# Kernel tuning notes

Hardware: AMD Instinct MI355X
Metric: run time of the kernel (lower is better)

Reference implementation:

```python
import jax, jax.numpy as jnp
import numpy as np

N, K, C, H, V = 4096, 32, 128, 128, 21   # residues, kNN, node/edge dim, hidden, vocab
NEG_SLOPE = 0.2

def gatv2(src_feat, tgt_feat, edge_feat, Wl, bl, Wr, br, We, be, att, b_out):
    # GATv2Conv (1 head, eval mode) on a regular kNN graph.
    # src_feat: [N,K,Din] gathered source-node features per edge; tgt_feat: [N,Din]
    xl = src_feat @ Wl + bl                       # [N,K,C]
    xr = tgt_feat @ Wr + br                       # [N,C]
    ee = edge_feat @ We + be                      # [N,K,C]
    m = jax.nn.leaky_relu(xl + xr[:, None, :] + ee, NEG_SLOPE)
    alpha = jax.nn.softmax(jnp.einsum('nkc,c->nk', m, att), axis=1)
    return jnp.einsum('nk,nkc->nc', alpha, xl) + b_out

def setup_inputs():
    key = jax.random.key(0)
    ks = jax.random.split(key, 32)
    w = lambda k, s: jax.random.normal(k, s, jnp.float32) * 0.05
    z0 = lambda s: jnp.zeros(s, jnp.float32)
    return dict(
        E=jax.random.normal(ks[0], (N, K, C), jnp.float32),
        E_idx=jax.random.randint(ks[1], (N, K), 0, N),
        S=jax.random.randint(ks[2], (N,), 0, V),
        mask=jnp.ones((N,), jnp.float32),
        chain_M=jnp.ones((N,), jnp.float32),
        z=jax.random.normal(ks[3], (N,), jnp.float32),
        Wl1=w(ks[4], (C, C)), bl1=z0((C,)),
        Wr1=w(ks[5], (C, C)), br1=z0((C,)),
        We1=w(ks[6], (C, C)), be1=z0((C,)),
        a1=w(ks[7], (C,)), bo1=z0((C,)),
        Wl2=w(ks[8], (C + H, C)), bl2=z0((C,)),
        Wr2=w(ks[9], (C + H, C)), br2=z0((C,)),
        We2=w(ks[10], (C, C)), be2=z0((C,)),
        a2=w(ks[11], (C,)), bo2=z0((C,)),
        W_s=w(ks[12], (V, H)),
        W_out=w(ks[13], (C, V)), b_out=z0((V,)),
    )

def reference(E, E_idx, S, mask, chain_M, z,
              Wl1, bl1, Wr1, br1, We1, be1, a1, bo1,
              Wl2, bl2, Wr2, br2, We2, be2, a2, bo2,
              W_s, W_out, b_out):
    # encoder GAT over zero-initialized node features
    x0 = jnp.zeros((N, C), E.dtype)
    node_attr = gatv2(x0[E_idx], x0, E, Wl1, bl1, Wr1, br1, We1, be1, a1, bo1)
    seq_attr = W_s[S]                                        # [N,H]
    h_full = jnp.concatenate([node_attr, seq_attr], -1)      # [N,C+H]
    h_mask = jnp.concatenate([node_attr, jnp.zeros_like(seq_attr)], -1)
    cm = chain_M * mask
    decoding_order = jnp.argsort((cm + 1e-4) * jnp.abs(z))   # [N]
    P = jax.nn.one_hot(decoding_order, N, dtype=E.dtype)     # [N,N] permutation
    L = 1.0 - jnp.triu(jnp.ones((N, N), E.dtype))            # strictly lower tri
    order_mask_backward = jnp.einsum('ij,iq,jp->qp', L, P, P)
    mask_attend = jnp.take_along_axis(order_mask_backward, E_idx, axis=1)[..., None]
    m1d = mask[:, None, None]
    mask_bw = m1d * mask_attend
    mask_fw = m1d * (1.0 - mask_attend)
    # per-edge source features: neighbor seq embedding visible only if decoded earlier
    src = h_full[E_idx] * mask_bw + h_mask[E_idx] * mask_fw  # [N,K,C+H]
    out = gatv2(src, h_mask, E, Wl2, bl2, Wr2, br2, We2, be2, a2, bo2)
    logits = out @ W_out + b_out
    return jax.nn.log_softmax(logits, axis=-1)
```

## Files before the change

### kernel.cpp

```cpp
#include <hip/hip_runtime.h>
#include <hip/hip_bf16.h>

typedef short short8 __attribute__((ext_vector_type(8)));
typedef float float4v __attribute__((ext_vector_type(4)));

#define WS_T   0
#define WS_D   2688
#define WS_C   2816
#define WS_O   2944
#define WS_A2  3072
#define WS_G   7296
#define WS_B0  7744
#define WS_B1  7776
#define WS_M   7808

__device__ __forceinline__ unsigned int pack2bf(float a, float b) {
  union { float f; unsigned int u; } xa, xb;
  xa.f = a; xb.f = b;
  return ((xa.u + 0x8000u) >> 16) | ((xb.u + 0x8000u) & 0xFFFF0000u);
}

__global__ __launch_bounds__(256) void pg10_pre(
    const float* __restrict__ Wl2, const float* __restrict__ Wr2,
    const float* __restrict__ We2, const float* __restrict__ bl1,
    const float* __restrict__ bl2, const float* __restrict__ br2,
    const float* __restrict__ be2, const float* __restrict__ a2,
    const float* __restrict__ bo1, const float* __restrict__ bo2,
    const float* __restrict__ W_s, const float* __restrict__ mask,
    const float* __restrict__ chain_M, const float* __restrict__ z,
    const int* __restrict__ S, const float* __restrict__ W_out,
    const float* __restrict__ b_out, void* __restrict__ ws)
{
  __shared__ float sA[128], sB[128];
  short* wsW = (short*)ws;
  float* F = (float*)ws + 8192;
  const int b = blockIdx.x, tid = threadIdx.x;
  if (b == 0) {
    for (int s = tid; s < 16384; s += 256) {
      const int row = s >> 7, c = s & 127;
      const int q = row >> 5, lh = (row & 31) >> 3, j = row & 7;
      const int t = c >> 4, cl = c & 15;
      union { float f; unsigned int u; } x; x.f = We2[s];
      const unsigned int r = x.u + 0x7FFFu + ((x.u >> 16) & 1u);
      wsW[(((q * 8 + t) * 64) + lh * 16 + cl) * 8 + j] = (short)(r >> 16);
    }
    if (tid < 128) {
      const int c = tid;
      float cl0 = 0.f, cr0 = 0.f;
      for (int i = 0; i < 128; i++) {
        const float s = bl1[i] + bo1[i];
        cl0 += s * Wl2[i * 128 + c];
        cr0 += s * Wr2[i * 128 + c];
      }
      const float O = bl2[c] + bo2[c];
      F[WS_D + c]  = be2[c] + bl2[c] + br2[c] + cr0;
      F[WS_C + c]  = cl0;
      F[WS_O + c]  = O;
      F[WS_A2 + c] = a2[c];
      sA[c] = O;
      sB[c] = cl0;
    }
    __syncthreads();
    if (tid < 21) {
      float b0 = b_out[tid], b1 = 0.f;
      for (int c = 0; c < 128; c++) {
        b0 = fmaf(sA[c], W_out[c * 21 + tid], b0);
        b1 = fmaf(sB[c], W_out[c * 21 + tid], b1);
      }
      F[WS_B0 + tid] = b0;
      F[WS_B1 + tid] = b1;
    }
  } else if (b <= 21) {
    const int v = b - 1;
    if (tid < 128) {
      const int c = tid;
      float acc = 0.f;
      for (int h = 0; h < 128; h++)
        acc += W_s[v * 128 + h] * Wl2[(128 + h) * 128 + c];
      F[WS_T + v * 128 + c] = acc;
      sA[c] = acc;
    }
    __syncthreads();
    if (tid < 21) {
      float g = 0.f;
      for (int c = 0; c < 128; c++)
        g = fmaf(sA[c], W_out[c * 21 + tid], g);
      F[WS_G + v * 21 + tid] = g;
    }
  } else {
    const int n = (b - 22) * 256 + tid;
    F[WS_M + 2 * n] = (chain_M[n] * mask[n] + 1e-4f) * fabsf(z[n]);
    ((int*)F)[WS_M + 2 * n + 1] = S[n];
  }
}

__global__ __launch_bounds__(256, 4) void pg10_main(
    const float* __restrict__ E, const int* __restrict__ E_idx,
    const float* __restrict__ mask, const void* __restrict__ ws,
    float* __restrict__ out)
{
  __shared__ __align__(16) short ldsE[4][32 * 136];

  const short* wsW = (const short*)ws;
  const float* F = (const float*)ws + 8192;
  const int tid  = threadIdx.x;
  const int wave = tid >> 6;
  const int lane = tid & 63;
  const int quad = lane >> 4;
  const int lid  = lane & 15;
  const int n    = blockIdx.x * 4 + wave;
  const float maskn = mask[n];

  int jidx = 0;
  if (lane < 32) jidx = E_idx[n * 32 + lane];

  const float* ebase = E + (size_t)n * 32 * 128;
  short* myE = ldsE[wave];
#pragma unroll
  for (int i = 0; i < 8; i++) {
    const int e = i * 512 + lane * 8;
    const float4 A = *(const float4*)(ebase + e);
    const float4 B = *(const float4*)(ebase + e + 4);
    union { short8 s; unsigned int u[4]; } v;
    v.u[0] = pack2bf(A.x, A.y);
    v.u[1] = pack2bf(A.z, A.w);
    v.u[2] = pack2bf(B.x, B.y);
    v.u[3] = pack2bf(B.z, B.w);
    *(short8*)(myE + (e >> 7) * 136 + (e & 127)) = v.s;
  }

  float wkv = 0.f; int rvv = 0;
  const float keyn = F[WS_M + 2 * n];
  if (lane < 32) {
    const float2 mj = *(const float2*)(F + WS_M + 2 * jidx);
    const int before = (mj.x < keyn) || (mj.x == keyn && jidx < n);
    wkv = before ? maskn : 0.f;
    union { float f; int i; } c; c.f = mj.y; rvv = c.i;
  }
  int rows[2][4]; float wks[2][4];
#pragma unroll
  for (int g = 0; g < 2; g++)
#pragma unroll
    for (int r = 0; r < 4; r++) {
      const int kk = g * 16 + quad * 4 + r;
      rows[g][r] = __shfl(rvv, kk) * 128;
      wks[g][r]  = __shfl(wkv, kk);
    }

  __builtin_amdgcn_wave_barrier();

  short8 afr[2][4];
#pragma unroll
  for (int g = 0; g < 2; g++)
#pragma unroll
    for (int q = 0; q < 4; q++)
      afr[g][q] = *(const short8*)(myE + (g * 16 + lid) * 136 + q * 32 + quad * 8);

  float part[2][4] = {{0.f, 0.f, 0.f, 0.f}, {0.f, 0.f, 0.f, 0.f}};
#pragma unroll
  for (int t = 0; t < 8; t++) {
    short8 bfr[4];
#pragma unroll
    for (int q = 0; q < 4; q++)
      bfr[q] = *(const short8*)(wsW + (((q * 8 + t) * 64) + lane) * 8);
    float4v ac0 = {0.f, 0.f, 0.f, 0.f}, ac1 = {0.f, 0.f, 0.f, 0.f};
#pragma unroll
    for (int q = 0; q < 4; q++) {
      ac0 = __builtin_amdgcn_mfma_f32_16x16x32_bf16(afr[0][q], bfr[q], ac0, 0, 0, 0);
      ac1 = __builtin_amdgcn_mfma_f32_16x16x32_bf16(afr[1][q], bfr[q], ac1, 0, 0, 0);
    }
    const int c = t * 16 + lid;
    const float dvt  = F[WS_D + c] + maskn * F[WS_C + c];
    const float a2vt = F[WS_A2 + c];
#pragma unroll
    for (int r = 0; r < 4; r++) {
      float v0 = ac0[r] + dvt + wks[0][r] * F[WS_T + rows[0][r] + c];
      float v1 = ac1[r] + dvt + wks[1][r] * F[WS_T + rows[1][r] + c];
      v0 = fmaxf(v0, 0.f) + 0.2f * fminf(v0, 0.f);
      v1 = fmaxf(v1, 0.f) + 0.2f * fminf(v1, 0.f);
      part[0][r] = fmaf(v0, a2vt, part[0][r]);
      part[1][r] = fmaf(v1, a2vt, part[1][r]);
    }
  }
  float sreg[2][4];
#pragma unroll
  for (int g = 0; g < 2; g++)
#pragma unroll
    for (int r = 0; r < 4; r++) {
      float v = part[g][r];
      v += __shfl_xor(v, 1);
      v += __shfl_xor(v, 2);
      v += __shfl_xor(v, 4);
      v += __shfl_xor(v, 8);
      sreg[g][r] = v;
    }

  float mx = -1e30f;
#pragma unroll
  for (int g = 0; g < 2; g++)
#pragma unroll
    for (int r = 0; r < 4; r++) mx = fmaxf(mx, sreg[g][r]);
  mx = fmaxf(mx, __shfl_xor(mx, 16));
  mx = fmaxf(mx, __shfl_xor(mx, 32));
  float eg[2][4], esum = 0.f;
#pragma unroll
  for (int g = 0; g < 2; g++)
#pragma unroll
    for (int r = 0; r < 4; r++) {
      eg[g][r] = expf(sreg[g][r] - mx);
      esum += eg[g][r];
    }
  esum += __shfl_xor(esum, 16);
  esum += __shfl_xor(esum, 32);
  const float inv = 1.f / esum;
  float cg[2][4];
#pragma unroll
  for (int g = 0; g < 2; g++)
#pragma unroll
    for (int r = 0; r < 4; r++) cg[g][r] = eg[g][r] * inv * wks[g][r];

  float lg = (lane < 21) ? (F[WS_B0 + lane] + maskn * F[WS_B1 + lane]) : -1e30f;
#pragma unroll
  for (int kk = 0; kk < 32; kk++) {
    const int g = kk >> 4, sq = (kk >> 2) & 3, r = kk & 3;
    const float cf = __shfl(cg[g][r], sq * 16);
    const int row = (rows[0][0], __shfl(rvv, kk)) * 21;
    if (lane < 21) lg = fmaf(cf, F[WS_G + row + lane], lg);
  }

  float lmx = lg;
  lmx = fmaxf(lmx, __shfl_xor(lmx, 1));
  lmx = fmaxf(lmx, __shfl_xor(lmx, 2));
  lmx = fmaxf(lmx, __shfl_xor(lmx, 4));
  lmx = fmaxf(lmx, __shfl_xor(lmx, 8));
  lmx = fmaxf(lmx, __shfl_xor(lmx, 16));
  float ex = (lane < 21) ? expf(lg - lmx) : 0.f;
  float es = ex;
  es += __shfl_xor(es, 1);
  es += __shfl_xor(es, 2);
  es += __shfl_xor(es, 4);
  es += __shfl_xor(es, 8);
  es += __shfl_xor(es, 16);
  if (lane < 21)
    out[n * 21 + lane] = lg - lmx - logf(es);
}

extern "C" void kernel_launch(void* const* d_in, const int* in_sizes, int n_in,
                              void* d_out, int out_size, void* d_ws, size_t ws_size,
                              hipStream_t stream)
{
  const float* E       = (const float*)d_in[0];
  const int*   E_idx   = (const int*)d_in[1];
  const int*   S       = (const int*)d_in[2];
  const float* mask    = (const float*)d_in[3];
  const float* chain_M = (const float*)d_in[4];
  const float* z       = (const float*)d_in[5];
  const float* bl1     = (const float*)d_in[7];
  const float* bo1     = (const float*)d_in[13];
  const float* Wl2     = (const float*)d_in[14];
  const float* bl2     = (const float*)d_in[15];
  const float* Wr2     = (const float*)d_in[16];
  const float* br2     = (const float*)d_in[17];
  const float* We2     = (const float*)d_in[18];
  const float* be2     = (const float*)d_in[19];
  const float* a2      = (const float*)d_in[20];
  const float* bo2     = (const float*)d_in[21];
  const float* W_s     = (const float*)d_in[22];
  const float* W_out   = (const float*)d_in[23];
  const float* b_out   = (const float*)d_in[24];

  pg10_pre<<<38, 256, 0, stream>>>(Wl2, Wr2, We2, bl1, bl2, br2, be2, a2,
                                   bo1, bo2, W_s, mask, chain_M, z, S,
                                   W_out, b_out, d_ws);
  pg10_main<<<1024, 256, 0, stream>>>(E, E_idx, mask, d_ws, (float*)d_out);
}
```

Before: 168.2 us.

## Use intrinsic bf16 packing, hoist per-channel constants, split logit accumulation

Replaces the hand-written round-half-up bf16 packing of E with the HIP __float22bfloat162_rn intrinsic, which rounds to nearest even and may map to a packed convert instruction. Hoists the per-channel bias and attention-vector loads out of the MFMA loop into register arrays. Splits the 32-step logit accumulation into two independent FMA chains to shorten the dependency chain. These add register pressure under a 4-blocks-per-SM launch bound, and the rounding change slightly alters numerics.

```diff
diff --git a/kernel.cpp b/kernel.cpp
--- a/kernel.cpp
+++ b/kernel.cpp
@@ -14,13 +14,18 @@
 #define WS_B1  7776
 #define WS_M   7808
 
-__device__ __forceinline__ unsigned int pack2bf(float a, float b) {
-  union { float f; unsigned int u; } xa, xb;
-  xa.f = a; xb.f = b;
-  return ((xa.u + 0x8000u) >> 16) | ((xb.u + 0x8000u) & 0xFFFF0000u);
-}
-
-__global__ __launch_bounds__(256) void pg10_pre(
+__device__ __forceinline__ ushort f2bf(float f) {
+  union { float f; unsigned int u; } x;
+  x.f = f;
+  unsigned int r = x.u + 0x7FFFu + ((x.u >> 16) & 1u);
+  return (ushort)(r >> 16);
+}
+__device__ __forceinline__ unsigned int pkbf(float a, float b) {
+  __hip_bfloat162 h = __float22bfloat162_rn(make_float2(a, b));
+  return *(unsigned int*)&h;
+}
+
+__global__ __launch_bounds__(256) void pg12_pre(
     const float* __restrict__ Wl2, const float* __restrict__ Wr2,
     const float* __restrict__ We2, const float* __restrict__ bl1,
     const float* __restrict__ bl2, const float* __restrict__ br2,
@@ -40,9 +45,7 @@
       const int row = s >> 7, c = s & 127;
       const int q = row >> 5, lh = (row & 31) >> 3, j = row & 7;
       const int t = c >> 4, cl = c & 15;
-      union { float f; unsigned int u; } x; x.f = We2[s];
-      const unsigned int r = x.u + 0x7FFFu + ((x.u >> 16) & 1u);
-      wsW[(((q * 8 + t) * 64) + lh * 16 + cl) * 8 + j] = (short)(r >> 16);
+      wsW[(((q * 8 + t) * 64) + lh * 16 + cl) * 8 + j] = (short)f2bf(We2[s]);
     }
     if (tid < 128) {
       const int c = tid;
@@ -94,7 +97,7 @@
   }
 }
 
-__global__ __launch_bounds__(256, 4) void pg10_main(
+__global__ __launch_bounds__(256, 4) void pg12_main(
     const float* __restrict__ E, const int* __restrict__ E_idx,
     const float* __restrict__ mask, const void* __restrict__ ws,
     float* __restrict__ out)
@@ -122,10 +125,10 @@
     const float4 A = *(const float4*)(ebase + e);
     const float4 B = *(const float4*)(ebase + e + 4);
     union { short8 s; unsigned int u[4]; } v;
-    v.u[0] = pack2bf(A.x, A.y);
-    v.u[1] = pack2bf(A.z, A.w);
-    v.u[2] = pack2bf(B.x, B.y);
-    v.u[3] = pack2bf(B.z, B.w);
+    v.u[0] = pkbf(A.x, A.y);
+    v.u[1] = pkbf(A.z, A.w);
+    v.u[2] = pkbf(B.x, B.y);
+    v.u[3] = pkbf(B.z, B.w);
     *(short8*)(myE + (e >> 7) * 136 + (e & 127)) = v.s;
   }
 
@@ -147,6 +150,14 @@
       wks[g][r]  = __shfl(wkv, kk);
     }
 
+  float dv[8], a2v[8];
+#pragma unroll
+  for (int t = 0; t < 8; t++) {
+    const int c = t * 16 + lid;
+    dv[t]  = F[WS_D + c] + maskn * F[WS_C + c];
+    a2v[t] = F[WS_A2 + c];
+  }
+
   __builtin_amdgcn_wave_barrier();
 
   short8 afr[2][4];
@@ -170,16 +181,14 @@
       ac1 = __builtin_amdgcn_mfma_f32_16x16x32_bf16(afr[1][q], bfr[q], ac1, 0, 0, 0);
     }
     const int c = t * 16 + lid;
-    const float dvt  = F[WS_D + c] + maskn * F[WS_C + c];
-    const float a2vt = F[WS_A2 + c];
-#pragma unroll
-    for (int r = 0; r < 4; r++) {
-      float v0 = ac0[r] + dvt + wks[0][r] * F[WS_T + rows[0][r] + c];
-      float v1 = ac1[r] + dvt + wks[1][r] * F[WS_T + rows[1][r] + c];
+#pragma unroll
+    for (int r = 0; r < 4; r++) {
+      float v0 = ac0[r] + dv[t] + wks[0][r] * F[WS_T + rows[0][r] + c];
+      float v1 = ac1[r] + dv[t] + wks[1][r] * F[WS_T + rows[1][r] + c];
       v0 = fmaxf(v0, 0.f) + 0.2f * fminf(v0, 0.f);
       v1 = fmaxf(v1, 0.f) + 0.2f * fminf(v1, 0.f);
-      part[0][r] = fmaf(v0, a2vt, part[0][r]);
-      part[1][r] = fmaf(v1, a2vt, part[1][r]);
+      part[0][r] = fmaf(v0, a2v[t], part[0][r]);
+      part[1][r] = fmaf(v1, a2v[t], part[1][r]);
     }
   }
   float sreg[2][4];
@@ -219,14 +228,23 @@
 #pragma unroll
     for (int r = 0; r < 4; r++) cg[g][r] = eg[g][r] * inv * wks[g][r];
 
-  float lg = (lane < 21) ? (F[WS_B0 + lane] + maskn * F[WS_B1 + lane]) : -1e30f;
-#pragma unroll
-  for (int kk = 0; kk < 32; kk++) {
-    const int g = kk >> 4, sq = (kk >> 2) & 3, r = kk & 3;
-    const float cf = __shfl(cg[g][r], sq * 16);
-    const int row = (rows[0][0], __shfl(rvv, kk)) * 21;
-    if (lane < 21) lg = fmaf(cf, F[WS_G + row + lane], lg);
-  }
+  float lg0 = (lane < 21) ? (F[WS_B0 + lane] + maskn * F[WS_B1 + lane]) : -1e30f;
+  float lg1 = 0.f;
+#pragma unroll
+  for (int kk = 0; kk < 32; kk += 2) {
+    const int g0 = kk >> 4, sq0 = (kk >> 2) & 3, r0 = kk & 3;
+    const int k1 = kk + 1;
+    const int g1 = k1 >> 4, sq1 = (k1 >> 2) & 3, r1 = k1 & 3;
+    const float cf0 = __shfl(cg[g0][r0], sq0 * 16);
+    const float cf1 = __shfl(cg[g1][r1], sq1 * 16);
+    const int row0 = __shfl(rvv, kk) * 21;
+    const int row1 = __shfl(rvv, k1) * 21;
+    if (lane < 21) {
+      lg0 = fmaf(cf0, F[WS_G + row0 + lane], lg0);
+      lg1 = fmaf(cf1, F[WS_G + row1 + lane], lg1);
+    }
+  }
+  const float lg = lg0 + lg1;
 
   float lmx = lg;
   lmx = fmaxf(lmx, __shfl_xor(lmx, 1));
@@ -269,8 +287,8 @@
   const float* W_out   = (const float*)d_in[23];
   const float* b_out   = (const float*)d_in[24];
 
-  pg10_pre<<<38, 256, 0, stream>>>(Wl2, Wr2, We2, bl1, bl2, br2, be2, a2,
+  pg12_pre<<<38, 256, 0, stream>>>(Wl2, Wr2, We2, bl1, bl2, br2, be2, a2,
                                    bo1, bo2, W_s, mask, chain_M, z, S,
                                    W_out, b_out, d_ws);
-  pg10_main<<<1024, 256, 0, stream>>>(E, E_idx, mask, d_ws, (float*)d_out);
-}
+  pg12_main<<<1024, 256, 0, stream>>>(E, E_idx, mask, d_ws, (float*)d_out);
+}
```

Result: no change. 171.0 us (+1.7%).
